# Optimization experiments

Hardware: AMD Instinct MI355X
Metric: run time of the kernel (lower is better)

## Reference

```python
import jax, jax.numpy as jnp
import numpy as np
import math


def _grid_sample_trilinear_zeros(x, grid):
    """Faithful port of F.grid_sample (5D, bilinear/trilinear, padding_mode='zeros',
    align_corners=False). x: [B,C,D,H,W]; grid: [D,H,W,3] with (x,y,z) normalized
    coords shared across the batch (theta is identical per batch element)."""
    B, C, D, H, W = x.shape
    # unnormalize (align_corners=False): ix = ((gx+1)*W - 1)/2
    ix = ((grid[..., 0] + 1.0) * W - 1.0) * 0.5
    iy = ((grid[..., 1] + 1.0) * H - 1.0) * 0.5
    iz = ((grid[..., 2] + 1.0) * D - 1.0) * 0.5
    ix0f = jnp.floor(ix); iy0f = jnp.floor(iy); iz0f = jnp.floor(iz)
    fx = ix - ix0f; fy = iy - iy0f; fz = iz - iz0f
    ix0 = ix0f.astype(jnp.int32); iy0 = iy0f.astype(jnp.int32); iz0 = iz0f.astype(jnp.int32)
    N = D * H * W
    x_flat = x.reshape(B, C, N)
    out = jnp.zeros((B, C, N), dtype=x.dtype)
    for dz in (0, 1):
        for dy in (0, 1):
            for dx in (0, 1):
                xi = ix0 + dx; yi = iy0 + dy; zi = iz0 + dz
                w = ((fx if dx else 1.0 - fx)
                     * (fy if dy else 1.0 - fy)
                     * (fz if dz else 1.0 - fz)).reshape(N)
                valid = ((xi >= 0) & (xi < W) & (yi >= 0) & (yi < H)
                         & (zi >= 0) & (zi < D)).reshape(N)
                lin = (jnp.clip(zi, 0, D - 1) * (H * W)
                       + jnp.clip(yi, 0, H - 1) * W
                       + jnp.clip(xi, 0, W - 1)).reshape(N)
                out = out + jnp.take(x_flat, lin, axis=2) * jnp.where(valid, w, 0.0).astype(x.dtype)
    return out  # [B,C,N]


def _angular_hallucination(x_cls, angle):
    B, C, H, W = x_cls.shape
    D = 1
    # NOTE: original uses math.cos(angle) with angle an integer (degrees-as-radians quirk)
    c = math.cos(angle); s = math.sin(angle)
    theta = jnp.array([[c, 0.0, s, 0.0],
                       [0.0, 1.0, 0.0, 0.0],
                       [-s, 0.0, c, 0.0]], dtype=x_cls.dtype)  # [3,4]
    # affine_grid base coords, align_corners=False: (2i+1)/size - 1
    xs = (2.0 * jnp.arange(W, dtype=x_cls.dtype) + 1.0) / W - 1.0
    ys = (2.0 * jnp.arange(H, dtype=x_cls.dtype) + 1.0) / H - 1.0
    zs = (2.0 * jnp.arange(D, dtype=x_cls.dtype) + 1.0) / D - 1.0
    gz, gy, gx = jnp.meshgrid(zs, ys, xs, indexing='ij')  # each [D,H,W]
    base = jnp.stack([gx, gy, gz, jnp.ones_like(gx)], axis=-1)  # [D,H,W,4] = (x,y,z,1)
    grid = jnp.einsum('dhwk,ik->dhwi', base, theta)  # [D,H,W,3]
    x_angular = _grid_sample_trilinear_zeros(x_cls[:, :, None], grid)  # [B,C,H*W]
    x_t = x_cls.reshape(B, C, H * W)
    # corr[b,i,j] = sum_n x_cls[b,i,n] * x_angular[b,j,n]
    corr = jnp.einsum('bin,bjn->bij', x_t, x_angular)  # [B,C,C]
    pro = jax.nn.softmax(corr, axis=1)  # softmax over dim=1 as in torch
    out = jnp.einsum('bij,bjn->bin', pro, x_t)
    return out.reshape(B, C, H, W)


def setup_inputs() -> dict:
    key = jax.random.key(0)
    x_cls = jax.random.normal(key, (8, 64, 256, 256), dtype=jnp.float32)
    return {"x_cls": x_cls, "angle": 45}


def reference(x_cls, angle):
    return _angular_hallucination(x_cls, angle)
```

## Files before the change

kernel.cpp:

```cpp
#include <hip/hip_runtime.h>
#include <math.h>

#define BB 8
#define CC 64
#define HH 256
#define WW 256
#define NN (HH*WW)
#define LDS_STRIDE 68
#define JCHUNK 4

__global__ __launch_bounds__(512, 4)
void corr_kernel(const float* __restrict__ x, const int* __restrict__ angle_p,
                 float* __restrict__ corr) {
    __shared__ float  Xs[WW][LDS_STRIDE];
    __shared__ float4 tbl[WW];

    const int jc  = blockIdx.x;
    const int b   = blockIdx.y;
    const int tid = threadIdx.x;

    if (tid < 256) {
        const double a  = (double)(*angle_p);
        const float  cf = (float)cos(a);
        const float  sf = (float)sin(a);
        const int i = tid;
        const float gx    = (2.0f * (float)i + 1.0f) / 256.0f - 1.0f;
        const float gridx = cf * gx;
        const float gridz = (-sf) * gx;
        const float ix = ((gridx + 1.0f) * 256.0f - 1.0f) * 0.5f;
        const float t1 = (gridz + 1.0f);
        const float iz = (t1 - 1.0f) * 0.5f;
        const float ix0f = floorf(ix), iz0f = floorf(iz);
        const float fx = ix - ix0f,    fz = iz - iz0f;
        const int   ix0 = (int)ix0f,   iz0 = (int)iz0f;
        float wz = 0.0f;
        if (iz0 ==  0) wz += 1.0f - fz;
        if (iz0 == -1) wz += fz;
        float w0 = (1.0f - fx) * wz;
        float w1 = fx * wz;
        int k0 = ix0, k1 = ix0 + 1;
        if (k0 < 0 || k0 >= WW) { w0 = 0.0f; k0 = 0; }
        if (k1 < 0 || k1 >= WW) { w1 = 0.0f; k1 = 0; }
        tbl[i] = make_float4(w0, w1, __int_as_float(k0), __int_as_float(k1));
    }

    const int w    = tid >> 6;
    const int lane = tid & 63;
    const int lr   = lane >> 3;
    const int lc   = lane & 7;

    float4 acc0[8], acc1[8];
    #pragma unroll
    for (int r = 0; r < 8; ++r) {
        acc0[r] = make_float4(0.f, 0.f, 0.f, 0.f);
        acc1[r] = make_float4(0.f, 0.f, 0.f, 0.f);
    }

    const int si = tid & 255;
    const int c0 = (tid >> 8) * 32;

    for (int jj = 0; jj < JCHUNK; ++jj) {
        const int j = jc * JCHUNK + jj;
        __syncthreads();
        {
            const float* xb = x + (size_t)(b * CC) * NN + (size_t)j * WW;
            #pragma unroll 16
            for (int cc = 0; cc < 32; ++cc)
                Xs[si][c0 + cc] = xb[(size_t)(c0 + cc) * NN + si];
        }
        __syncthreads();

        const int ib = 32 * w;
        float4 tv = tbl[ib];
        for (int ii = 0; ii < 32; ++ii) {
            const int i = ib + ii;
            const float4 tn = tbl[(i + 1) & 255];
            const int   k0 = __float_as_int(tv.z);
            const int   k1 = __float_as_int(tv.w);
            const float w0 = tv.x, w1 = tv.y;

            const float4 xpa = *(const float4*)&Xs[i][8 * lr];
            const float4 xpb = *(const float4*)&Xs[i][8 * lr + 4];
            const float4 a0  = *(const float4*)&Xs[k0][8 * lc];
            const float4 a1  = *(const float4*)&Xs[k0][8 * lc + 4];
            const float4 b0  = *(const float4*)&Xs[k1][8 * lc];
            const float4 b1  = *(const float4*)&Xs[k1][8 * lc + 4];

            float4 y0, y1;
            y0.x = fmaf(w1, b0.x, w0 * a0.x);
            y0.y = fmaf(w1, b0.y, w0 * a0.y);
            y0.z = fmaf(w1, b0.z, w0 * a0.z);
            y0.w = fmaf(w1, b0.w, w0 * a0.w);
            y1.x = fmaf(w1, b1.x, w0 * a1.x);
            y1.y = fmaf(w1, b1.y, w0 * a1.y);
            y1.z = fmaf(w1, b1.z, w0 * a1.z);
            y1.w = fmaf(w1, b1.w, w0 * a1.w);

            const float xp[8] = {xpa.x, xpa.y, xpa.z, xpa.w,
                                 xpb.x, xpb.y, xpb.z, xpb.w};
            #pragma unroll
            for (int r = 0; r < 8; ++r) {
                acc0[r].x = fmaf(xp[r], y0.x, acc0[r].x);
                acc0[r].y = fmaf(xp[r], y0.y, acc0[r].y);
                acc0[r].z = fmaf(xp[r], y0.z, acc0[r].z);
                acc0[r].w = fmaf(xp[r], y0.w, acc0[r].w);
                acc1[r].x = fmaf(xp[r], y1.x, acc1[r].x);
                acc1[r].y = fmaf(xp[r], y1.y, acc1[r].y);
                acc1[r].z = fmaf(xp[r], y1.z, acc1[r].z);
                acc1[r].w = fmaf(xp[r], y1.w, acc1[r].w);
            }
            tv = tn;
        }
    }

    float4* S4 = (float4*)&Xs[0][0];
    const int idx0 = (8 * lr) * 16 + 2 * lc;

    __syncthreads();
    if (w >= 4) {
        float4* dst = S4 + (size_t)(w - 4) * 1024;
        #pragma unroll
        for (int r = 0; r < 8; ++r) {
            dst[idx0 + 16 * r]     = acc0[r];
            dst[idx0 + 16 * r + 1] = acc1[r];
        }
    }
    __syncthreads();
    if (w < 4) {
        const float4* src = S4 + (size_t)w * 1024;
        #pragma unroll
        for (int r = 0; r < 8; ++r) {
            const float4 u = src[idx0 + 16 * r];
            const float4 v = src[idx0 + 16 * r + 1];
            acc0[r].x += u.x; acc0[r].y += u.y; acc0[r].z += u.z; acc0[r].w += u.w;
            acc1[r].x += v.x; acc1[r].y += v.y; acc1[r].z += v.z; acc1[r].w += v.w;
        }
    }
    __syncthreads();
    if (w == 2 || w == 3) {
        float4* dst = S4 + (size_t)(w - 2) * 1024;
        #pragma unroll
        for (int r = 0; r < 8; ++r) {
            dst[idx0 + 16 * r]     = acc0[r];
            dst[idx0 + 16 * r + 1] = acc1[r];
        }
    }
    __syncthreads();
    if (w < 2) {
        const float4* src = S4 + (size_t)w * 1024;
        #pragma unroll
        for (int r = 0; r < 8; ++r) {
            const float4 u = src[idx0 + 16 * r];
            const float4 v = src[idx0 + 16 * r + 1];
            acc0[r].x += u.x; acc0[r].y += u.y; acc0[r].z += u.z; acc0[r].w += u.w;
            acc1[r].x += v.x; acc1[r].y += v.y; acc1[r].z += v.z; acc1[r].w += v.w;
        }
    }
    __syncthreads();
    if (w == 1) {
        #pragma unroll
        for (int r = 0; r < 8; ++r) {
            S4[idx0 + 16 * r]     = acc0[r];
            S4[idx0 + 16 * r + 1] = acc1[r];
        }
    }
    __syncthreads();
    if (w == 0) {
        #pragma unroll
        for (int r = 0; r < 8; ++r) {
            const float4 u = S4[idx0 + 16 * r];
            const float4 v = S4[idx0 + 16 * r + 1];
            acc0[r].x += u.x; acc0[r].y += u.y; acc0[r].z += u.z; acc0[r].w += u.w;
            acc1[r].x += v.x; acc1[r].y += v.y; acc1[r].z += v.z; acc1[r].w += v.w;
        }
        float* cb = corr + (size_t)b * CC * CC;
        #pragma unroll
        for (int r = 0; r < 8; ++r) {
            const int off = (8 * lr + r) * CC + 8 * lc;
            atomicAdd(&cb[off + 0], acc0[r].x);
            atomicAdd(&cb[off + 1], acc0[r].y);
            atomicAdd(&cb[off + 2], acc0[r].z);
            atomicAdd(&cb[off + 3], acc0[r].w);
            atomicAdd(&cb[off + 4], acc1[r].x);
            atomicAdd(&cb[off + 5], acc1[r].y);
            atomicAdd(&cb[off + 6], acc1[r].z);
            atomicAdd(&cb[off + 7], acc1[r].w);
        }
    }
}

__global__ void softmax_kernel(const float* __restrict__ corr,
                               float* __restrict__ proT) {
    const int b  = blockIdx.x;
    const int jj = threadIdx.x;
    const float* cb = corr + (size_t)b * CC * CC;
    float v[CC];
    float m = -1e30f;
    #pragma unroll
    for (int i = 0; i < CC; ++i) {
        v[i] = cb[i * CC + jj];
        m = fmaxf(m, v[i]);
    }
    float ssum = 0.0f;
    #pragma unroll
    for (int i = 0; i < CC; ++i) {
        v[i] = expf(v[i] - m);
        ssum += v[i];
    }
    const float inv = 1.0f / ssum;
    float* pb = proT + (size_t)b * CC * CC + (size_t)jj * CC;
    #pragma unroll
    for (int i = 0; i < CC; ++i) pb[i] = v[i] * inv;
}

__global__ __launch_bounds__(512, 4)
void apply_kernel(const float* __restrict__ x, const float* __restrict__ proT,
                  float* __restrict__ out) {
    __shared__ float P[CC * CC];
    const int b   = blockIdx.y;
    const int n0  = blockIdx.x * 256;
    const int tid = threadIdx.x;
    for (int t = tid; t < CC * CC; t += 512)
        P[t] = proT[(size_t)b * CC * CC + t];
    __syncthreads();

    const int lane = tid & 63;
    const int w    = tid >> 6;
    const float* xb = x + (size_t)b * CC * NN + n0 + 4 * lane;

    float4 acc[8];
    #pragma unroll
    for (int r = 0; r < 8; ++r) acc[r] = make_float4(0.f, 0.f, 0.f, 0.f);

    float4 buf[4];
    #pragma unroll
    for (int u = 0; u < 4; ++u) buf[u] = *(const float4*)(xb + (size_t)u * NN);

    #pragma unroll 4
    for (int q = 0; q < CC; ++q) {
        const float4 xv = buf[q & 3];
        if (q + 4 < CC) buf[q & 3] = *(const float4*)(xb + (size_t)(q + 4) * NN);

        const float4 pa = *(const float4*)&P[q * CC + 8 * w];
        const float4 pb = *(const float4*)&P[q * CC + 8 * w + 4];
        const float pv[8] = {pa.x, pa.y, pa.z, pa.w, pb.x, pb.y, pb.z, pb.w};
        #pragma unroll
        for (int r = 0; r < 8; ++r) {
            acc[r].x = fmaf(pv[r], xv.x, acc[r].x);
            acc[r].y = fmaf(pv[r], xv.y, acc[r].y);
            acc[r].z = fmaf(pv[r], xv.z, acc[r].z);
            acc[r].w = fmaf(pv[r], xv.w, acc[r].w);
        }
    }

    float* ob = out + (size_t)b * CC * NN + n0 + 4 * lane;
    #pragma unroll
    for (int r = 0; r < 8; ++r) {
        *(float4*)(ob + (size_t)(8 * w + r) * NN) = acc[r];
    }
}

extern "C" void kernel_launch(void* const* d_in, const int* in_sizes, int n_in,
                              void* d_out, int out_size, void* d_ws, size_t ws_size,
                              hipStream_t stream) {
    const float* x     = (const float*)d_in[0];
    const int*   angle = (const int*)d_in[1];
    float*       out   = (float*)d_out;

    float* corr = (float*)d_ws;
    float* proT = corr + (size_t)BB * CC * CC;

    (void)hipMemsetAsync(d_ws, 0, (size_t)BB * CC * CC * sizeof(float), stream);

    corr_kernel<<<dim3(HH / JCHUNK, BB), 512, 0, stream>>>(x, angle, corr);
    softmax_kernel<<<dim3(BB), dim3(CC), 0, stream>>>(corr, proT);
    apply_kernel<<<dim3(NN / 256, BB), 512, 0, stream>>>(x, proT, out);
}
```

Before: 439.8 us.

## Double-buffer LDS row tiles with vectorized register prefetch and readlane weight tables

Global loads now fetch float4 rows per channel into registers one row ahead, stored transposed into a double-buffered LDS tile with a swizzled column layout. The intent is to overlap global memory latency with the FMA loop and replace the old scalar strided gather. The per-column interpolation weights and indices are kept in registers and broadcast with readlane instead of read from an LDS table. JCHUNK grows to 8, and the larger LDS footprint lowers launch bounds occupancy to 2 blocks, which may reduce latency hiding.

```diff
diff --git a/kernel.cpp b/kernel.cpp
--- a/kernel.cpp
+++ b/kernel.cpp
@@ -7,24 +7,41 @@
 #define WW 256
 #define NN (HH*WW)
 #define LDS_STRIDE 68
-#define JCHUNK 4
-
-__global__ __launch_bounds__(512, 4)
+#define JCHUNK 8
+
+__device__ __forceinline__ int colw(int c) {
+    const int cb = c >> 2;
+    const int col4 = (cb >> 1) | ((cb & 1) << 3);
+    return col4 * 4 + (c & 3);
+}
+
+__device__ __forceinline__ float rlf(float v, int l) {
+    return __int_as_float(__builtin_amdgcn_readlane(__float_as_int(v), l));
+}
+
+__global__ __launch_bounds__(512, 2)
 void corr_kernel(const float* __restrict__ x, const int* __restrict__ angle_p,
                  float* __restrict__ corr) {
-    __shared__ float  Xs[WW][LDS_STRIDE];
-    __shared__ float4 tbl[WW];
+    __shared__ float Xs[2][HH][LDS_STRIDE];
 
     const int jc  = blockIdx.x;
     const int b   = blockIdx.y;
     const int tid = threadIdx.x;
-
-    if (tid < 256) {
+    const int J0  = jc * JCHUNK;
+
+    const int w    = tid >> 6;
+    const int lane = tid & 63;
+    const int lr   = lane >> 3;
+    const int lc   = lane & 7;
+    const int ib   = 32 * w;
+
+    float tw0, tw1; int tk0, tk1;
+    {
         const double a  = (double)(*angle_p);
         const float  cf = (float)cos(a);
         const float  sf = (float)sin(a);
-        const int i = tid;
-        const float gx    = (2.0f * (float)i + 1.0f) / 256.0f - 1.0f;
+        const int it = ib + (lane & 31);
+        const float gx    = (2.0f * (float)it + 1.0f) / 256.0f - 1.0f;
         const float gridx = cf * gx;
         const float gridz = (-sf) * gx;
         const float ix = ((gridx + 1.0f) * 256.0f - 1.0f) * 0.5f;
@@ -41,13 +58,31 @@
         int k0 = ix0, k1 = ix0 + 1;
         if (k0 < 0 || k0 >= WW) { w0 = 0.0f; k0 = 0; }
         if (k1 < 0 || k1 >= WW) { w1 = 0.0f; k1 = 0; }
-        tbl[i] = make_float4(w0, w1, __int_as_float(k0), __int_as_float(k1));
-    }
-
-    const int w    = tid >> 6;
-    const int lane = tid & 63;
-    const int lr   = lane >> 3;
-    const int lc   = lane & 7;
+        tw0 = w0; tw1 = w1; tk0 = k0; tk1 = k1;
+    }
+
+    const int sc   = tid & 63;
+    const int sw   = tid >> 6;
+    const int scol = colw(sc);
+    const float* xrow = x + ((size_t)b * CC + sc) * NN;
+
+    float4 sreg[8];
+
+    #pragma unroll
+    for (int v = 0; v < 8; ++v)
+        sreg[v] = *(const float4*)(xrow + (size_t)J0 * WW + 4 * (sw + 8 * v));
+    #pragma unroll
+    for (int v = 0; v < 8; ++v) {
+        const int u = sw + 8 * v;
+        Xs[0][4*u+0][scol] = sreg[v].x;
+        Xs[0][4*u+1][scol] = sreg[v].y;
+        Xs[0][4*u+2][scol] = sreg[v].z;
+        Xs[0][4*u+3][scol] = sreg[v].w;
+    }
+    #pragma unroll
+    for (int v = 0; v < 8; ++v)
+        sreg[v] = *(const float4*)(xrow + (size_t)(J0 + 1) * WW + 4 * (sw + 8 * v));
+    __syncthreads();
 
     float4 acc0[8], acc1[8];
     #pragma unroll
@@ -56,35 +91,43 @@
         acc1[r] = make_float4(0.f, 0.f, 0.f, 0.f);
     }
 
-    const int si = tid & 255;
-    const int c0 = (tid >> 8) * 32;
-
     for (int jj = 0; jj < JCHUNK; ++jj) {
-        const int j = jc * JCHUNK + jj;
-        __syncthreads();
-        {
-            const float* xb = x + (size_t)(b * CC) * NN + (size_t)j * WW;
-            #pragma unroll 16
-            for (int cc = 0; cc < 32; ++cc)
-                Xs[si][c0 + cc] = xb[(size_t)(c0 + cc) * NN + si];
-        }
-        __syncthreads();
-
-        const int ib = 32 * w;
-        float4 tv = tbl[ib];
+        const int cur = jj & 1;
+
+        if (jj < JCHUNK - 1) {
+            #pragma unroll
+            for (int v = 0; v < 8; ++v) {
+                const int u = sw + 8 * v;
+                Xs[cur ^ 1][4*u+0][scol] = sreg[v].x;
+                Xs[cur ^ 1][4*u+1][scol] = sreg[v].y;
+                Xs[cur ^ 1][4*u+2][scol] = sreg[v].z;
+                Xs[cur ^ 1][4*u+3][scol] = sreg[v].w;
+            }
+        }
+        if (jj < JCHUNK - 2) {
+            #pragma unroll
+            for (int v = 0; v < 8; ++v)
+                sreg[v] = *(const float4*)(xrow + (size_t)(J0 + jj + 2) * WW + 4 * (sw + 8 * v));
+        }
+
+        const float* Xc = &Xs[cur][0][0];
+        #pragma unroll 4
         for (int ii = 0; ii < 32; ++ii) {
-            const int i = ib + ii;
-            const float4 tn = tbl[(i + 1) & 255];
-            const int   k0 = __float_as_int(tv.z);
-            const int   k1 = __float_as_int(tv.w);
-            const float w0 = tv.x, w1 = tv.y;
-
-            const float4 xpa = *(const float4*)&Xs[i][8 * lr];
-            const float4 xpb = *(const float4*)&Xs[i][8 * lr + 4];
-            const float4 a0  = *(const float4*)&Xs[k0][8 * lc];
-            const float4 a1  = *(const float4*)&Xs[k0][8 * lc + 4];
-            const float4 b0  = *(const float4*)&Xs[k1][8 * lc];
-            const float4 b1  = *(const float4*)&Xs[k1][8 * lc + 4];
+            const float w0 = rlf(tw0, ii);
+            const float w1 = rlf(tw1, ii);
+            const int   k0 = __builtin_amdgcn_readlane(tk0, ii);
+            const int   k1 = __builtin_amdgcn_readlane(tk1, ii);
+
+            const float* rowP = Xc + (ib + ii) * LDS_STRIDE;
+            const float* rowA = Xc + k0 * LDS_STRIDE;
+            const float* rowB = Xc + k1 * LDS_STRIDE;
+
+            const float4 xpa = *(const float4*)(rowP + 4 * lr);
+            const float4 xpb = *(const float4*)(rowP + 4 * lr + 32);
+            const float4 a0  = *(const float4*)(rowA + 4 * lc);
+            const float4 a1  = *(const float4*)(rowA + 4 * lc + 32);
+            const float4 b0  = *(const float4*)(rowB + 4 * lc);
+            const float4 b1  = *(const float4*)(rowB + 4 * lc + 32);
 
             float4 y0, y1;
             y0.x = fmaf(w1, b0.x, w0 * a0.x);
@@ -109,14 +152,13 @@
                 acc1[r].z = fmaf(xp[r], y1.z, acc1[r].z);
                 acc1[r].w = fmaf(xp[r], y1.w, acc1[r].w);
             }
-            tv = tn;
-        }
-    }
-
-    float4* S4 = (float4*)&Xs[0][0];
+        }
+        __syncthreads();
+    }
+
+    float4* S4 = (float4*)&Xs[0][0][0];
     const int idx0 = (8 * lr) * 16 + 2 * lc;
 
-    __syncthreads();
     if (w >= 4) {
         float4* dst = S4 + (size_t)(w - 4) * 1024;
         #pragma unroll
```

Result: faster. 364.6 us (-17.1%).
